# Optimization experiments

Hardware: AMD Instinct MI355X
Metric: run time of the kernel (lower is better)

Reference implementation:

```python
import jax, jax.numpy as jnp
import numpy as np

N = 10000
E = 160000
NEG_SLOPE = 0.2
BN_EPS = 1e-5


def _gat_conv(x, W, a_src, a_dst, b, src, dst, n, heads):
    # PyG GATConv, concat=False (mean over heads), shared lin for src/dst.
    H = heads
    C = W.shape[1] // H
    h = (x @ W).reshape(n, H, C)                       # (N,H,C)
    e_s = jnp.einsum('nhc,hc->nh', h, a_src)           # (N,H)
    e_d = jnp.einsum('nhc,hc->nh', h, a_dst)
    alpha = jax.nn.leaky_relu(e_s[src] + e_d[dst], NEG_SLOPE)   # (E',H)
    amax = jax.ops.segment_max(alpha, dst, num_segments=n)       # per-dst softmax
    ex = jnp.exp(alpha - amax[dst])
    denom = jax.ops.segment_sum(ex, dst, num_segments=n)
    w = ex / (denom[dst] + 1e-16)
    out = jax.ops.segment_sum(h[src] * w[:, :, None], dst, num_segments=n)  # (N,H,C)
    return out.mean(axis=1) + b


def _bn(x, g, b):
    mu = x.mean(axis=0)
    var = x.var(axis=0)  # biased, as torch BN training forward
    return (x - mu) * jax.lax.rsqrt(var + BN_EPS) * g + b


def setup_inputs() -> dict:
    key = jax.random.key(0)
    ks = jax.random.split(key, 32)
    d = {}
    d['x'] = jax.random.normal(ks[0], (N, 64), jnp.float32)
    d['edge_index'] = jax.random.randint(ks[1], (2, E), 0, N, jnp.int64)
    s = lambda k, shape, fan: jax.random.normal(k, shape, jnp.float32) * (1.0 / np.sqrt(fan))
    d['Wp'] = s(ks[2], (64, 128), 64); d['bp'] = jnp.zeros((128,), jnp.float32)
    # conv0: 8 heads, per-head 128
    d['W0'] = s(ks[3], (128, 8 * 128), 128); d['as0'] = s(ks[4], (8, 128), 128)
    d['ad0'] = s(ks[5], (8, 128), 128); d['b0'] = jnp.zeros((128,), jnp.float32)
    d['g0'] = jnp.ones((128,), jnp.float32); d['be0'] = jnp.zeros((128,), jnp.float32)
    # conv1: same shape
    d['W1'] = s(ks[6], (128, 8 * 128), 128); d['as1'] = s(ks[7], (8, 128), 128)
    d['ad1'] = s(ks[8], (8, 128), 128); d['b1'] = jnp.zeros((128,), jnp.float32)
    d['g1'] = jnp.ones((128,), jnp.float32); d['be1'] = jnp.zeros((128,), jnp.float32)
    # conv2: 1 head, out 64
    d['W2'] = s(ks[9], (128, 64), 128); d['as2'] = s(ks[10], (1, 64), 64)
    d['ad2'] = s(ks[11], (1, 64), 64); d['b2'] = jnp.zeros((64,), jnp.float32)
    d['g2'] = jnp.ones((64,), jnp.float32); d['be2'] = jnp.zeros((64,), jnp.float32)
    # residual projection for layer 2 (128 -> 64)
    d['Wr'] = s(ks[12], (128, 64), 128); d['br'] = jnp.zeros((64,), jnp.float32)
    return d


def reference(x, edge_index, Wp, bp, W0, as0, ad0, b0, g0, be0,
              W1, as1, ad1, b1, g1, be1, W2, as2, ad2, b2, g2, be2, Wr, br):
    n = x.shape[0]
    loops = jnp.arange(n, dtype=edge_index.dtype)
    src = jnp.concatenate([edge_index[0], loops])  # add_self_loops=True
    dst = jnp.concatenate([edge_index[1], loops])
    h = x @ Wp + bp
    # layer 0 (8 heads, identity residual)
    hr = h
    h = jax.nn.elu(_bn(_gat_conv(h, W0, as0, ad0, b0, src, dst, n, 8), g0, be0)) + hr
    # layer 1
    hr = h
    h = jax.nn.elu(_bn(_gat_conv(h, W1, as1, ad1, b1, src, dst, n, 8), g1, be1)) + hr
    # layer 2 (1 head, linear residual 128->64)
    hr = h @ Wr + br
    h = jax.nn.elu(_bn(_gat_conv(h, W2, as2, ad2, b2, src, dst, n, 1), g2, be2)) + hr
    return h
```

## Files before the change

### kernel.cpp

```cpp
#include <hip/hip_runtime.h>
#include <hip/hip_bf16.h>
#include <cstdint>
#include <cstddef>

#define TPB 256

typedef __attribute__((ext_vector_type(8))) short bf16x8;
typedef __attribute__((ext_vector_type(8))) unsigned short ushort8;
typedef __attribute__((ext_vector_type(4))) float f32x4;

static __device__ __forceinline__ float bf2f(unsigned short u) {
  union { unsigned int i; float f; } c;
  c.i = ((unsigned int)u) << 16;
  return c.f;
}

__global__ void detect_kernel(const unsigned int* __restrict__ w, int* __restrict__ flag) {
  __shared__ int any32;
  if (threadIdx.x == 0) any32 = 0;
  __syncthreads();
  for (int i = threadIdx.x; i < 1024; i += TPB)
    if (w[2 * i + 1] != 0u) any32 = 1;
  __syncthreads();
  if (threadIdx.x == 0) *flag = any32;
}

__global__ void decode_kernel(const void* __restrict__ raw, const int* __restrict__ flag,
                              int* __restrict__ src, int* __restrict__ dst, int E, int n) {
  int i = blockIdx.x * TPB + threadIdx.x;
  int tot = E + n;
  if (i >= tot) return;
  if (i < E) {
    if (*flag) {
      const int* p = (const int*)raw;
      src[i] = p[i];
      dst[i] = p[E + i];
    } else {
      const long long* p = (const long long*)raw;
      src[i] = (int)p[i];
      dst[i] = (int)p[E + i];
    }
  } else {
    src[i] = i - E;
    dst[i] = i - E;
  }
}

__global__ void count_kernel(const int* __restrict__ dst, int* __restrict__ counts, int etot) {
  int i = blockIdx.x * TPB + threadIdx.x;
  if (i < etot) atomicAdd(&counts[dst[i]], 1);
}

__global__ void scan_kernel(const int* __restrict__ counts, int* __restrict__ row_ptr, int n) {
  __shared__ int part[TPB];
  int tid = threadIdx.x;
  int chunk = (n + TPB - 1) / TPB;
  int begin = tid * chunk;
  int end = begin + chunk; if (end > n) end = n;
  int s = 0;
  for (int i = begin; i < end && i < n; i++) s += counts[i];
  part[tid] = s;
  __syncthreads();
  for (int off = 1; off < TPB; off <<= 1) {
    int v = (tid >= off) ? part[tid - off] : 0;
    __syncthreads();
    part[tid] += v;
    __syncthreads();
  }
  int base = (tid == 0) ? 0 : part[tid - 1];
  for (int i = begin; i < end && i < n; i++) { row_ptr[i] = base; base += counts[i]; }
  if (tid == TPB - 1) row_ptr[n] = base;
}

__global__ void fill_kernel(const int* __restrict__ src, const int* __restrict__ dst,
                            const int* __restrict__ row_ptr, int* __restrict__ fill,
                            int* __restrict__ sorted_src, int etot) {
  int i = blockIdx.x * TPB + threadIdx.x;
  if (i >= etot) return;
  int d = dst[i];
  int pos = row_ptr[d] + atomicAdd(&fill[d], 1);
  sorted_src[pos] = src[i];
}

__global__ void f32_to_bf16_kernel(const float* __restrict__ in, __hip_bfloat16* __restrict__ out, int n) {
  int i = blockIdx.x * TPB + threadIdx.x;
  if (i < n) out[i] = __float2bfloat16(in[i]);
}

__global__ void f32_to_bf16_T_kernel(const float* __restrict__ in, __hip_bfloat16* __restrict__ out,
                                     int K, int N) {
  __shared__ float tile[32][33];
// ... 28 lines not shown
  f32x4 acc[8];
#pragma unroll
  for (int nt = 0; nt < 8; nt++) acc[nt] = (f32x4){0.f, 0.f, 0.f, 0.f};

  const int arow = tid >> 2;
  const int akk = (tid & 3) << 3;
  const int brow = tid >> 1;
  const int bkk = (tid & 1) << 4;

  for (int k0 = 0; k0 < K; k0 += 32) {
    {
      int gr = bm + arow;
      if (gr < M) {
        *(bf16x8*)&As[arow][akk] = *(const bf16x8*)&A[(size_t)gr * K + k0 + akk];
      } else {
        bf16x8 z = {0, 0, 0, 0, 0, 0, 0, 0};
        *(bf16x8*)&As[arow][akk] = z;
      }
    }
    {
      int gbn = bn + brow;
      if (gbn < Ncols) {
        const short* bp = &Bt[(size_t)gbn * K + k0 + bkk];
        *(bf16x8*)&Bs[brow][bkk]     = *(const bf16x8*)bp;
        *(bf16x8*)&Bs[brow][bkk + 8] = *(const bf16x8*)(bp + 8);
      } else {
        bf16x8 z = {0, 0, 0, 0, 0, 0, 0, 0};
        *(bf16x8*)&Bs[brow][bkk] = z;
        *(bf16x8*)&Bs[brow][bkk + 8] = z;
      }
    }
    __syncthreads();

    bf16x8 a = *(const bf16x8*)&As[w * 16 + (lane & 15)][(lane >> 4) * 8];
#pragma unroll
    for (int nt = 0; nt < 8; nt++) {
      bf16x8 b = *(const bf16x8*)&Bs[nt * 16 + (lane & 15)][(lane >> 4) * 8];
      acc[nt] = __builtin_amdgcn_mfma_f32_16x16x32_bf16(a, b, acc[nt], 0, 0, 0);
    }
    __syncthreads();
  }

  float p1[4] = {0.f, 0.f, 0.f, 0.f};
  float p2[4] = {0.f, 0.f, 0.f, 0.f};

#pragma unroll
  for (int nt = 0; nt < 8; nt++) {
    int gc = bn + nt * 16 + (lane & 15);
    if (gc >= Ncols) continue;
    float bv = bias ? bias[gc] : 0.f;
    float asv = es_out ? asrc[gc] : 0.f;
    float adv = es_out ? adst[gc] : 0.f;
#pragma unroll
    for (int q = 0; q < 4; q++) {
      int gr = bm + w * 16 + (lane >> 4) * 4 + q;
      if (gr < M) {
        float val = acc[nt][q] + bv;
        if (C) C[(size_t)gr * Ncols + gc] = val;
        if (Cb) Cb[(size_t)gr * Ncols + gc] = __float2bfloat16(val);
        p1[q] += val * asv;
        p2[q] += val * adv;
      }
    }
  }

  if (es_out) {
    const int head = bn >> hshift;
#pragma unroll
    for (int q = 0; q < 4; q++) {
      float s1 = p1[q], s2 = p2[q];
      s1 += __shfl_xor(s1, 1); s2 += __shfl_xor(s2, 1);
      s1 += __shfl_xor(s1, 2); s2 += __shfl_xor(s2, 2);
      s1 += __shfl_xor(s1, 4); s2 += __shfl_xor(s2, 4);
      s1 += __shfl_xor(s1, 8); s2 += __shfl_xor(s2, 8);
      int gr = bm + w * 16 + (lane >> 4) * 4 + q;
      if ((lane & 15) == 0 && gr < M) {
        es_out[(size_t)gr * H + head] = s1;
        ed_out[(size_t)gr * H + head] = s2;
      }
    }
  }
}

__global__ __launch_bounds__(256) void gat_aggregate8w_kernel(
    const int* __restrict__ row_ptr, const int* __restrict__ srcs,
    const unsigned short* __restrict__ gb, const float* __restrict__ es,
    const float* __restrict__ ed, const float* __restrict__ bias,
    float* __restrict__ out, int n) {
  const int wave = threadIdx.x >> 6;
  const int lane = threadIdx.x & 63;
  const int v = blockIdx.x * 4 + wave;

  __shared__ float wlds[4][64][8];
  __shared__ int slds[4][64];

  if (v >= n) return;

  const int begin = row_ptr[v];
  const int deg = row_ptr[v + 1] - begin;

  const int eh = lane & 7;
  const int ee = lane >> 3;
  const int hh = lane >> 3;
  const int c0 = lane << 4;

  const float edv = ed[(size_t)v * 8 + eh];

  float acc[16];
#pragma unroll
  for (int k = 0; k < 16; k++) acc[k] = 0.f;

  if (deg <= 64) {
    float a[8];
    int sreg[8];
#pragma unroll
    for (int b = 0; b < 8; b++) {
      a[b] = -1e30f;
      sreg[b] = 0;
      int e = b * 8 + ee;
      if (e < deg) {
        int s = srcs[begin + e];
        sreg[b] = s;
        float t = es[(size_t)s * 8 + eh] + edv;
        a[b] = t > 0.f ? t : 0.2f * t;
      }
    }
    float m = a[0];
#pragma unroll
    for (int b = 1; b < 8; b++) m = fmaxf(m, a[b]);
    m = fmaxf(m, __shfl_xor(m, 8));
    m = fmaxf(m, __shfl_xor(m, 16));
    m = fmaxf(m, __shfl_xor(m, 32));
    float dsum = 0.f;
#pragma unroll
    for (int b = 0; b < 8; b++) { a[b] = __expf(a[b] - m); dsum += a[b]; }
    dsum += __shfl_xor(dsum, 8);
    dsum += __shfl_xor(dsum, 16);
    dsum += __shfl_xor(dsum, 32);
    const float invd = 1.0f / (dsum + 1e-16f);
#pragma unroll
    for (int b = 0; b < 8; b++) {
      wlds[wave][b * 8 + ee][eh] = a[b] * invd;
      if (eh == 0) slds[wave][b * 8 + ee] = sreg[b];
    }

    const int npad = (deg + 3) & ~3;
    for (int j0 = 0; j0 < npad; j0 += 4) {
      float w0 = wlds[wave][j0 + 0][hh];
      float w1 = wlds[wave][j0 + 1][hh];
      float w2 = wlds[wave][j0 + 2][hh];
      float w3 = wlds[wave][j0 + 3][hh];
      int s0 = slds[wave][j0 + 0];
      int s1 = slds[wave][j0 + 1];
      int s2 = slds[wave][j0 + 2];
      int s3 = slds[wave][j0 + 3];
      const ushort8* p0 = (const ushort8*)&gb[(size_t)s0 * 1024 + c0];
      const ushort8* p1 = (const ushort8*)&gb[(size_t)s1 * 1024 + c0];
      const ushort8* p2 = (const ushort8*)&gb[(size_t)s2 * 1024 + c0];
      const ushort8* p3 = (const ushort8*)&gb[(size_t)s3 * 1024 + c0];
      ushort8 u0a = p0[0], u0b = p0[1];
      ushort8 u1a = p1[0], u1b = p1[1];
      ushort8 u2a = p2[0], u2b = p2[1];
      ushort8 u3a = p3[0], u3b = p3[1];
#pragma unroll
      for (int k = 0; k < 8; k++) {
        acc[k]     += w0 * bf2f(u0a[k]) + w1 * bf2f(u1a[k]) + w2 * bf2f(u2a[k]) + w3 * bf2f(u3a[k]);
        acc[k + 8] += w0 * bf2f(u0b[k]) + w1 * bf2f(u1b[k]) + w2 * bf2f(u2b[k]) + w3 * bf2f(u3b[k]);
      }
    }
  } else {
    float m = -1e30f;
    for (int base = ee; base < deg; base += 8) {
      int s = srcs[begin + base];
      float t = es[(size_t)s * 8 + eh] + edv;
      t = t > 0.f ? t : 0.2f * t;
      m = fmaxf(m, t);
    }
    m = fmaxf(m, __shfl_xor(m, 8));
    m = fmaxf(m, __shfl_xor(m, 16));
    m = fmaxf(m, __shfl_xor(m, 32));
    float dsum = 0.f;
    for (int base = ee; base < deg; base += 8) {
      int s = srcs[begin + base];
      float t = es[(size_t)s * 8 + eh] + edv;
      t = t > 0.f ? t : 0.2f * t;
      dsum += __expf(t - m);
    }
    dsum += __shfl_xor(dsum, 8);
    dsum += __shfl_xor(dsum, 16);
    dsum += __shfl_xor(dsum, 32);
    const float invd = 1.0f / (dsum + 1e-16f);

    for (int base = 0; base < deg; base += 64) {
      const int cnt = min(64, deg - base);
#pragma unroll
      for (int b = 0; b < 8; b++) {
        int e = base + b * 8 + ee;
        float wv = 0.f;
        int s = 0;
        if (e < deg) {
          s = srcs[begin + e];
          float t = es[(size_t)s * 8 + eh] + edv;
          t = t > 0.f ? t : 0.2f * t;
          wv = __expf(t - m) * invd;
        }
        wlds[wave][b * 8 + ee][eh] = wv;
        if (eh == 0) slds[wave][b * 8 + ee] = s;
      }
      const int npad = (cnt + 3) & ~3;
      for (int j0 = 0; j0 < npad; j0 += 4) {
        float w0 = wlds[wave][j0 + 0][hh];
        float w1 = wlds[wave][j0 + 1][hh];
        float w2 = wlds[wave][j0 + 2][hh];
        float w3 = wlds[wave][j0 + 3][hh];
        int s0 = slds[wave][j0 + 0];
        int s1 = slds[wave][j0 + 1];
        int s2 = slds[wave][j0 + 2];
        int s3 = slds[wave][j0 + 3];
        const ushort8* p0 = (const ushort8*)&gb[(size_t)s0 * 1024 + c0];
        const ushort8* p1 = (const ushort8*)&gb[(size_t)s1 * 1024 + c0];
        const ushort8* p2 = (const ushort8*)&gb[(size_t)s2 * 1024 + c0];
        const ushort8* p3 = (const ushort8*)&gb[(size_t)s3 * 1024 + c0];
        ushort8 u0a = p0[0], u0b = p0[1];
        ushort8 u1a = p1[0], u1b = p1[1];
        ushort8 u2a = p2[0], u2b = p2[1];
        ushort8 u3a = p3[0], u3b = p3[1];
#pragma unroll
        for (int k = 0; k < 8; k++) {
          acc[k]     += w0 * bf2f(u0a[k]) + w1 * bf2f(u1a[k]) + w2 * bf2f(u2a[k]) + w3 * bf2f(u3a[k]);
          acc[k + 8] += w0 * bf2f(u0b[k]) + w1 * bf2f(u1b[k]) + w2 * bf2f(u2b[k]) + w3 * bf2f(u3b[k]);
        }
      }
    }
  }

#pragma unroll
  for (int k = 0; k < 16; k++) {
    acc[k] += __shfl_xor(acc[k], 8);
    acc[k] += __shfl_xor(acc[k], 16);
    acc[k] += __shfl_xor(acc[k], 32);
  }
  if (hh == 0) {
    const int cc = (lane & 7) << 4;
#pragma unroll
    for (int k = 0; k < 16; k++)
      out[(size_t)v * 128 + cc + k] = acc[k] * 0.125f + bias[cc + k];
  }
}

__global__ __launch_bounds__(256) void gat_aggregate1_kernel(
    const int* __restrict__ row_ptr, const int* __restrict__ srcs,
    const float* __restrict__ g, const float* __restrict__ es,
    const float* __restrict__ ed, const float* __restrict__ bias,
    float* __restrict__ out, int n) {
  const int wave = threadIdx.x >> 6;
  const int lane = threadIdx.x & 63;
  const int v = blockIdx.x * 4 + wave;
  if (v >= n) return;

  const int begin = row_ptr[v];
  const int deg = row_ptr[v + 1] - begin;
  const float edv = ed[v];

  float pm = -1e30f;
  for (int j = lane; j < deg; j += 64) {
    float a = es[srcs[begin + j]] + edv;
    a = a > 0.f ? a : 0.2f * a;
    pm = fmaxf(pm, a);
  }
#pragma unroll
  for (int off = 32; off > 0; off >>= 1) pm = fmaxf(pm, __shfl_xor(pm, off));

  float ps = 0.f;
  for (int j = lane; j < deg; j += 64) {
    float a = es[srcs[begin + j]] + edv;
    a = a > 0.f ? a : 0.2f * a;
    ps += expf(a - pm);
  }
#pragma unroll
  for (int off = 32; off > 0; off >>= 1) ps += __shfl_xor(ps, off);
  const float invd = 1.0f / (ps + 1e-16f);

  float acc = 0.f;
  for (int base = 0; base < deg; base += 64) {
    int cnt = deg - base; if (cnt > 64) cnt = 64;
    int sv = 0; float wv = 0.f;
    if (lane < cnt) {
      sv = srcs[begin + base + lane];
      float a = es[sv] + edv;
      a = a > 0.f ? a : 0.2f * a;
      wv = expf(a - pm) * invd;
    }
    for (int j = 0; j < cnt; j++) {
      int s = __shfl(sv, j);
      float wgt = __shfl(wv, j);
      acc += wgt * g[(size_t)s * 64 + lane];
    }
  }
  out[(size_t)v * 64 + lane] = acc + bias[lane];
}

template <int C>
__global__ void bn_stats_kernel(const float* __restrict__ x, int n, float* __restrict__ sums) {
  constexpr int T = 256;
  constexpr int RPI = T / C;
  constexpr int ITER = 64;
  constexpr int ROWS = RPI * ITER;
  int c = threadIdx.x % C;
  int r0 = threadIdx.x / C;
  int rowBase = blockIdx.x * ROWS;
  float s = 0.f, q = 0.f;
  for (int it = 0; it < ITER; ++it) {
    int r = rowBase + it * RPI + r0;
    if (r < n) {
      float v = x[(size_t)r * C + c];
      s += v; q += v * v;
    }
  }
  __shared__ float ls[T], lq[T];
  ls[threadIdx.x] = s; lq[threadIdx.x] = q;
  __syncthreads();
  if (threadIdx.x < C) {
    float ts = 0.f, tq = 0.f;
    for (int r = 0; r < RPI; ++r) { ts += ls[c + r * C]; tq += lq[c + r * C]; }
    atomicAdd(&sums[c], ts);
    atomicAdd(&sums[C + c], tq);
  }
}

template <int C>
__global__ void bn_elu_res_kernel(const float* __restrict__ x, const float* __restrict__ sums,
                                  const float* __restrict__ gamma, const float* __restrict__ beta,
                                  const float* __restrict__ res, float* __restrict__ out,
                                  __hip_bfloat16* __restrict__ outb, int n) {
  int i = blockIdx.x * TPB + threadIdx.x;
  if (i >= n * C) return;
  int c = i % C;
  float inv_n = 1.0f / (float)n;
  float mu = sums[c] * inv_n;
  float var = sums[C + c] * inv_n - mu * mu;
  float y = (x[i] - mu) * rsqrtf(var + 1e-5f) * gamma[c] + beta[c];
  y = y > 0.f ? y : expm1f(y);
  y += res[i];
  out[i] = y;
  if (outb) outb[i] = __float2bfloat16(y);
}

extern "C" void kernel_launch(void* const* d_in, const int* in_sizes, int n_in,
                              void* d_out, int out_size, void* d_ws, size_t ws_size,
                              hipStream_t stream) {
  const float* x   = (const float*)d_in[0];
  const void*  ei  = d_in[1];
  const float* Wp  = (const float*)d_in[2];
  const float* bp  = (const float*)d_in[3];
  const float* W0  = (const float*)d_in[4];
  const float* as0 = (const float*)d_in[5];
  const float* ad0 = (const float*)d_in[6];
  const float* b0  = (const float*)d_in[7];
  const float* g0  = (const float*)d_in[8];
  const float* be0 = (const float*)d_in[9];
  const float* W1  = (const float*)d_in[10];
  const float* as1 = (const float*)d_in[11];
  const float* ad1 = (const float*)d_in[12];
  const float* b1  = (const float*)d_in[13];
  const float* g1  = (const float*)d_in[14];
  const float* be1 = (const float*)d_in[15];
  const float* W2  = (const float*)d_in[16];
  const float* as2 = (const float*)d_in[17];
  const float* ad2 = (const float*)d_in[18];
  const float* b2  = (const float*)d_in[19];
  const float* g2  = (const float*)d_in[20];
  const float* be2 = (const float*)d_in[21];
  const float* Wr  = (const float*)d_in[22];
  const float* br  = (const float*)d_in[23];

  const int N = in_sizes[0] / 64;
  const int E = in_sizes[1] / 2;
  const int ETOT = E + N;

  char* wsp = (char*)d_ws;
  size_t off = 0;
  auto alloc = [&](size_t bytes) -> void* {
    void* p = wsp + off;
    off += (bytes + 255) & ~(size_t)255;
    return p;
  };
  int*   flag    = (int*)alloc(4);
  int*   e_src   = (int*)alloc((size_t)ETOT * 4);
  int*   e_dst   = (int*)alloc((size_t)ETOT * 4);
  int*   counts  = (int*)alloc((size_t)N * 4);
  int*   fillc   = (int*)alloc((size_t)N * 4);
  int*   row_ptr = (int*)alloc((size_t)(N + 1) * 4);
  int*   s_src   = (int*)alloc((size_t)ETOT * 4);
  float* hA      = (float*)alloc((size_t)N * 128 * 4);
  float* hB      = (float*)alloc((size_t)N * 128 * 4);
  float* gbuf    = (float*)alloc((size_t)N * 64 * 4);
  float* gat     = (float*)alloc((size_t)N * 128 * 4);
  float* es      = (float*)alloc((size_t)N * 8 * 4);
  float* ed      = (float*)alloc((size_t)N * 8 * 4);
  float* bnsum   = (float*)alloc(2 * 128 * 4);
  __hip_bfloat16* gbufb = (__hip_bfloat16*)alloc((size_t)N * 1024 * 2);
  __hip_bfloat16* xb  = (__hip_bfloat16*)alloc((size_t)N * 64 * 2);
  __hip_bfloat16* hAb = (__hip_bfloat16*)alloc((size_t)N * 128 * 2);
  __hip_bfloat16* hBb = (__hip_bfloat16*)alloc((size_t)N * 128 * 2);
  __hip_bfloat16* WpT = (__hip_bfloat16*)alloc((size_t)128 * 64 * 2);
  __hip_bfloat16* W0T = (__hip_bfloat16*)alloc((size_t)1024 * 128 * 2);
  __hip_bfloat16* W1T = (__hip_bfloat16*)alloc((size_t)1024 * 128 * 2);
  __hip_bfloat16* W2T = (__hip_bfloat16*)alloc((size_t)64 * 128 * 2);
  __hip_bfloat16* WrT = (__hip_bfloat16*)alloc((size_t)64 * 128 * 2);

  const int egrid = (ETOT + TPB - 1) / TPB;
  const int mgrid = (N + 63) / 64;
  auto cgrid = [](int n) { return (n + TPB - 1) / TPB; };

  detect_kernel<<<1, TPB, 0, stream>>>((const unsigned int*)ei, flag);
  decode_kernel<<<egrid, TPB, 0, stream>>>(ei, flag, e_src, e_dst, E, N);
  hipMemsetAsync(counts, 0, (size_t)N * 4, stream);
  hipMemsetAsync(fillc, 0, (size_t)N * 4, stream);
  count_kernel<<<egrid, TPB, 0, stream>>>(e_dst, counts, ETOT);
  scan_kernel<<<1, TPB, 0, stream>>>(counts, row_ptr, N);
  fill_kernel<<<egrid, TPB, 0, stream>>>(e_src, e_dst, row_ptr, fillc, s_src, ETOT);

  f32_to_bf16_kernel<<<cgrid(N * 64), TPB, 0, stream>>>(x, xb, N * 64);
  f32_to_bf16_T_kernel<<<dim3(2, 4), 256, 0, stream>>>(Wp, WpT, 64, 128);
  f32_to_bf16_T_kernel<<<dim3(4, 32), 256, 0, stream>>>(W0, W0T, 128, 1024);
  f32_to_bf16_T_kernel<<<dim3(4, 32), 256, 0, stream>>>(W1, W1T, 128, 1024);
  f32_to_bf16_T_kernel<<<dim3(4, 2), 256, 0, stream>>>(W2, W2T, 128, 64);
  f32_to_bf16_T_kernel<<<dim3(4, 2), 256, 0, stream>>>(Wr, WrT, 128, 64);

  gemm_bf16t_kernel<<<dim3(mgrid, 1), 256, 0, stream>>>(
      (const short*)xb, (const short*)WpT, bp, hA, hAb, N, 128, 64,
      nullptr, nullptr, nullptr, nullptr, 1, 7);

  gemm_bf16t_kernel<<<dim3(mgrid, 8), 256, 0, stream>>>(
      (const short*)hAb, (const short*)W0T, nullptr, nullptr, gbufb, N, 1024, 128,
      as0, ad0, es, ed, 8, 7);
  gat_aggregate8w_kernel<<<(N + 3) / 4, 256, 0, stream>>>(
      row_ptr, s_src, (const unsigned short*)gbufb, es, ed, b0, gat, N);
  hipMemsetAsync(bnsum, 0, 2 * 128 * 4, stream);
  bn_stats_kernel<128><<<(N + 127) / 128, 256, 0, stream>>>(gat, N, bnsum);
  bn_elu_res_kernel<128><<<cgrid(N * 128), TPB, 0, stream>>>(gat, bnsum, g0, be0, hA, hB, hBb, N);

  gemm_bf16t_kernel<<<dim3(mgrid, 8), 256, 0, stream>>>(
      (const short*)hBb, (const short*)W1T, nullptr, nullptr, gbufb, N, 1024, 128,
      as1, ad1, es, ed, 8, 7);
  gat_aggregate8w_kernel<<<(N + 3) / 4, 256, 0, stream>>>(
      row_ptr, s_src, (const unsigned short*)gbufb, es, ed, b1, gat, N);
  hipMemsetAsync(bnsum, 0, 2 * 128 * 4, stream);
  bn_stats_kernel<128><<<(N + 127) / 128, 256, 0, stream>>>(gat, N, bnsum);
  bn_elu_res_kernel<128><<<cgrid(N * 128), TPB, 0, stream>>>(gat, bnsum, g1, be1, hB, hA, hAb, N);

  gemm_bf16t_kernel<<<dim3(mgrid, 1), 256, 0, stream>>>(
      (const short*)hAb, (const short*)WrT, br, hB, nullptr, N, 64, 128,
      nullptr, nullptr, nullptr, nullptr, 1, 7);
  gemm_bf16t_kernel<<<dim3(mgrid, 1), 256, 0, stream>>>(
      (const short*)hAb, (const short*)W2T, nullptr, gbuf, nullptr, N, 64, 128,
      as2, ad2, es, ed, 1, 6);
  gat_aggregate1_kernel<<<(N + 3) / 4, 256, 0, stream>>>(row_ptr, s_src, gbuf, es, ed, b2, gat, N);
  hipMemsetAsync(bnsum, 0, 2 * 64 * 4, stream);
  bn_stats_kernel<64><<<(N + 255) / 256, 256, 0, stream>>>(gat, N, bnsum);
  bn_elu_res_kernel<64><<<cgrid(N * 64), TPB, 0, stream>>>(gat, bnsum, g2, be2, hB, (float*)d_out, nullptr, N);
}
```

Measured before the change: 321.2 us.

## Split 8-head GAT aggregation across two waves per node, 4 heads each

The 8-head aggregation kernel now assigns two waves per destination node, each handling four heads (512 bf16 columns), so each lane accumulates 8 values instead of 16. The gather loop is unrolled to eight neighbours per step with a tree-shaped sum, and the two half-node partials are combined through shared memory after a block barrier. This aims to double the parallelism and memory-level concurrency of the gather-bound aggregation and to cut register pressure. It adds an LDS exchange and __syncthreads, and inactive waves must stay alive until the barrier. The single-head kernel also switches expf to __expf.

Result: no change. 319.8 us (-0.4%).

```diff
diff --git a/kernel.cpp b/kernel.cpp
--- a/kernel.cpp
+++ b/kernel.cpp
@@ -206,105 +206,113 @@
     const unsigned short* __restrict__ gb, const float* __restrict__ es,
     const float* __restrict__ ed, const float* __restrict__ bias,
     float* __restrict__ out, int n) {
-  const int wave = threadIdx.x >> 6;
+  const int wg = threadIdx.x >> 6;
   const int lane = threadIdx.x & 63;
-  const int v = blockIdx.x * 4 + wave;
-
-  __shared__ float wlds[4][64][8];
+  const int v = blockIdx.x * 2 + (wg >> 1);
+  const int w = wg & 1;
+
+  __shared__ float wlds[4][64][4];
   __shared__ int slds[4][64];
-
-  if (v >= n) return;
-
-  const int begin = row_ptr[v];
-  const int deg = row_ptr[v + 1] - begin;
-
-  const int eh = lane & 7;
-  const int ee = lane >> 3;
-  const int hh = lane >> 3;
-  const int c0 = lane << 4;
-
-  const float edv = ed[(size_t)v * 8 + eh];
-
-  float acc[16];
-#pragma unroll
-  for (int k = 0; k < 16; k++) acc[k] = 0.f;
-
-  if (deg <= 64) {
-    float a[8];
-    int sreg[8];
-#pragma unroll
-    for (int b = 0; b < 8; b++) {
+  __shared__ float plds[4][16][8];
+
+  const bool active = (v < n);
+  const int begin = active ? row_ptr[v] : 0;
+  const int deg = active ? (row_ptr[v + 1] - begin) : 0;
+
+  const int eh4 = lane & 3;
+  const int ee16 = lane >> 2;
+  const int hh4 = lane >> 4;
+  const int c0 = w * 512 + lane * 8;
+
+  const float edv = active ? ed[(size_t)v * 8 + w * 4 + eh4] : 0.f;
+
+  float acc[8];
+#pragma unroll
+  for (int k = 0; k < 8; k++) acc[k] = 0.f;
+
+  if (active && deg <= 64) {
+    float a[4];
+    int sreg[4];
+#pragma unroll
+    for (int b = 0; b < 4; b++) {
       a[b] = -1e30f;
       sreg[b] = 0;
-      int e = b * 8 + ee;
+      int e = b * 16 + ee16;
       if (e < deg) {
         int s = srcs[begin + e];
         sreg[b] = s;
-        float t = es[(size_t)s * 8 + eh] + edv;
+        float t = es[(size_t)s * 8 + w * 4 + eh4] + edv;
         a[b] = t > 0.f ? t : 0.2f * t;
       }
     }
-    float m = a[0];
-#pragma unroll
-    for (int b = 1; b < 8; b++) m = fmaxf(m, a[b]);
+    float m = fmaxf(fmaxf(a[0], a[1]), fmaxf(a[2], a[3]));
+    m = fmaxf(m, __shfl_xor(m, 4));
     m = fmaxf(m, __shfl_xor(m, 8));
     m = fmaxf(m, __shfl_xor(m, 16));
     m = fmaxf(m, __shfl_xor(m, 32));
     float dsum = 0.f;
 #pragma unroll
-    for (int b = 0; b < 8; b++) { a[b] = __expf(a[b] - m); dsum += a[b]; }
+    for (int b = 0; b < 4; b++) { a[b] = __expf(a[b] - m); dsum += a[b]; }
+    dsum += __shfl_xor(dsum, 4);
     dsum += __shfl_xor(dsum, 8);
     dsum += __shfl_xor(dsum, 16);
     dsum += __shfl_xor(dsum, 32);
     const float invd = 1.0f / (dsum + 1e-16f);
 #pragma unroll
-    for (int b = 0; b < 8; b++) {
-      wlds[wave][b * 8 + ee][eh] = a[b] * invd;
-      if (eh == 0) slds[wave][b * 8 + ee] = sreg[b];
-    }
-
-    const int npad = (deg + 3) & ~3;
-    for (int j0 = 0; j0 < npad; j0 += 4) {
-      float w0 = wlds[wave][j0 + 0][hh];
-      float w1 = wlds[wave][j0 + 1][hh];
-      float w2 = wlds[wave][j0 + 2][hh];
-      float w3 = wlds[wave][j0 + 3][hh];
-      int s0 = slds[wave][j0 + 0];
-      int s1 = slds[wave][j0 + 1];
-      int s2 = slds[wave][j0 + 2];
-      int s3 = slds[wave][j0 + 3];
-      const ushort8* p0 = (const ushort8*)&gb[(size_t)s0 * 1024 + c0];
-      const ushort8* p1 = (const ushort8*)&gb[(size_t)s1 * 1024 + c0];
-      const ushort8* p2 = (const ushort8*)&gb[(size_t)s2 * 1024 + c0];
-      const ushort8* p3 = (const ushort8*)&gb[(size_t)s3 * 1024 + c0];
-      ushort8 u0a = p0[0], u0b = p0[1];
-      ushort8 u1a = p1[0], u1b = p1[1];
-      ushort8 u2a = p2[0], u2b = p2[1];
-      ushort8 u3a = p3[0], u3b = p3[1];
+    for (int b = 0; b < 4; b++) {
+      wlds[wg][b * 16 + ee16][eh4] = a[b] * invd;
+      if (eh4 == 0) slds[wg][b * 16 + ee16] = sreg[b];
+    }
+
+#pragma unroll
+    for (int g8 = 0; g8 < 8; g8++) {
+      const int j0 = g8 * 8;
+      if (j0 >= deg) break;
+      float w0 = wlds[wg][j0 + 0][hh4], w1 = wlds[wg][j0 + 1][hh4];
+      float w2 = wlds[wg][j0 + 2][hh4], w3 = wlds[wg][j0 + 3][hh4];
+      float w4 = wlds[wg][j0 + 4][hh4], w5 = wlds[wg][j0 + 5][hh4];
+      float w6 = wlds[wg][j0 + 6][hh4], w7 = wlds[wg][j0 + 7][hh4];
+      int s0 = slds[wg][j0 + 0], s1 = slds[wg][j0 + 1];
+      int s2 = slds[wg][j0 + 2], s3 = slds[wg][j0 + 3];
+      int s4 = slds[wg][j0 + 4], s5 = slds[wg][j0 + 5];
+      int s6 = slds[wg][j0 + 6], s7 = slds[wg][j0 + 7];
+      ushort8 u0 = *(const ushort8*)&gb[(size_t)s0 * 1024 + c0];
+      ushort8 u1 = *(const ushort8*)&gb[(size_t)s1 * 1024 + c0];
+      ushort8 u2 = *(const ushort8*)&gb[(size_t)s2 * 1024 + c0];
+      ushort8 u3 = *(const ushort8*)&gb[(size_t)s3 * 1024 + c0];
+      ushort8 u4 = *(const ushort8*)&gb[(size_t)s4 * 1024 + c0];
+      ushort8 u5 = *(const ushort8*)&gb[(size_t)s5 * 1024 + c0];
+      ushort8 u6 = *(const ushort8*)&gb[(size_t)s6 * 1024 + c0];
+      ushort8 u7 = *(const ushort8*)&gb[(size_t)s7 * 1024 + c0];
 #pragma unroll
       for (int k = 0; k < 8; k++) {
-        acc[k]     += w0 * bf2f(u0a[k]) + w1 * bf2f(u1a[k]) + w2 * bf2f(u2a[k]) + w3 * bf2f(u3a[k]);
-        acc[k + 8] += w0 * bf2f(u0b[k]) + w1 * bf2f(u1b[k]) + w2 * bf2f(u2b[k]) + w3 * bf2f(u3b[k]);
-      }
-    }
-  } else {
+        float t0 = w0 * bf2f(u0[k]) + w1 * bf2f(u1[k]);
+        float t1 = w2 * bf2f(u2[k]) + w3 * bf2f(u3[k]);
+        float t2 = w4 * bf2f(u4[k]) + w5 * bf2f(u5[k]);
+        float t3 = w6 * bf2f(u6[k]) + w7 * bf2f(u7[k]);
+        acc[k] += (t0 + t1) + (t2 + t3);
+      }
+    }
+  } else if (active) {
     float m = -1e30f;
-    for (int base = ee; base < deg; base += 8) {
-      int s = srcs[begin + base];
-      float t = es[(size_t)s * 8 + eh] + edv;
+    for (int e = ee16; e < deg; e += 16) {
+      int s = srcs[begin + e];
+      float t = es[(size_t)s * 8 + w * 4 + eh4] + edv;
       t = t > 0.f ? t : 0.2f * t;
       m = fmaxf(m, t);
     }
+    m = fmaxf(m, __shfl_xor(m, 4));
     m = fmaxf(m, __shfl_xor(m, 8));
     m = fmaxf(m, __shfl_xor(m, 16));
     m = fmaxf(m, __shfl_xor(m, 32));
     float dsum = 0.f;
-    for (int base = ee; base < deg; base += 8) {
-      int s = srcs[begin + base];
-      float t = es[(size_t)s * 8 + eh] + edv;
+    for (int e = ee16; e < deg; e += 16) {
+      int s = srcs[begin + e];
+      float t = es[(size_t)s * 8 + w * 4 + eh4] + edv;
       t = t > 0.f ? t : 0.2f * t;
       dsum += __expf(t - m);
     }
+    dsum += __shfl_xor(dsum, 4);
     dsum += __shfl_xor(dsum, 8);
     dsum += __shfl_xor(dsum, 16);
     dsum += __shfl_xor(dsum, 32);
@@ -313,57 +321,67 @@
     for (int base = 0; base < deg; base += 64) {
       const int cnt = min(64, deg - base);
 #pragma unroll
-      for (int b = 0; b < 8; b++) {
-        int e = base + b * 8 + ee;
-        float wv = 0.f;
-        int s = 0;
+      for (int b = 0; b < 4; b++) {
+        int e = base + b * 16 + ee16;
+        float wv = 0.f; int s = 0;
         if (e < deg) {
           s = srcs[begin + e];
-          float t = es[(size_t)s * 8 + eh] + edv;
+          float t = es[(size_t)s * 8 + w * 4 + eh4] + edv;
           t = t > 0.f ? t : 0.2f * t;
           wv = __expf(t - m) * invd;
         }
-        wlds[wave][b * 8 + ee][eh] = wv;
-        if (eh == 0) slds[wave][b * 8 + ee] = s;
-      }
-      const int npad = (cnt + 3) & ~3;
-      for (int j0 = 0; j0 < npad; j0 += 4) {
-        float w0 = wlds[wave][j0 + 0][hh];
-        float w1 = wlds[wave][j0 + 1][hh];
-        float w2 = wlds[wave][j0 + 2][hh];
-        float w3 = wlds[wave][j0 + 3][hh];
-        int s0 = slds[wave][j0 + 0];
-        int s1 = slds[wave][j0 + 1];
-        int s2 = slds[wave][j0 + 2];
-        int s3 = slds[wave][j0 + 3];
-        const ushort8* p0 = (const ushort8*)&gb[(size_t)s0 * 1024 + c0];
-        const ushort8* p1 = (const ushort8*)&gb[(size_t)s1 * 1024 + c0];
-        const ushort8* p2 = (const ushort8*)&gb[(size_t)s2 * 1024 + c0];
-        const ushort8* p3 = (const ushort8*)&gb[(size_t)s3 * 1024 + c0];
-        ushort8 u0a = p0[0], u0b = p0[1];
-        ushort8 u1a = p1[0], u1b = p1[1];
-        ushort8 u2a = p2[0], u2b = p2[1];
-        ushort8 u3a = p3[0], u3b = p3[1];
+        wlds[wg][b * 16 + ee16][eh4] = wv;
+        if (eh4 == 0) slds[wg][b * 16 + ee16] = s;
+      }
+#pragma unroll
+      for (int g8 = 0; g8 < 8; g8++) {
+        const int j0 = g8 * 8;
+        if (j0 >= cnt) break;
+        float w0 = wlds[wg][j0 + 0][hh4], w1 = wlds[wg][j0 + 1][hh4];
+        float w2 = wlds[wg][j0 + 2][hh4], w3 = wlds[wg][j0 + 3][hh4];
+        float w4 = wlds[wg][j0 + 4][hh4], w5 = wlds[wg][j0 + 5][hh4];
+        float w6 = wlds[wg][j0 + 6][hh4], w7 = wlds[wg][j0 + 7][hh4];
+        int s0 = slds[wg][j0 + 0], s1 = slds[wg][j0 + 1];
+        int s2 = slds[wg][j0 + 2], s3 = slds[wg][j0 + 3];
+        int s4 = slds[wg][j0 + 4], s5 = slds[wg][j0 + 5];
+        int s6 = slds[wg][j0 + 6], s7 = slds[wg][j0 + 7];
+        ushort8 u0 = *(const ushort8*)&gb[(size_t)s0 * 1024 + c0];
+        ushort8 u1 = *(const ushort8*)&gb[(size_t)s1 * 1024 + c0];
+        ushort8 u2 = *(const ushort8*)&gb[(size_t)s2 * 1024 + c0];
+        ushort8 u3 = *(const ushort8*)&gb[(size_t)s3 * 1024 + c0];
+        ushort8 u4 = *(const ushort8*)&gb[(size_t)s4 * 1024 + c0];
+        ushort8 u5 = *(const ushort8*)&gb[(size_t)s5 * 1024 + c0];
+        ushort8 u6 = *(const ushort8*)&gb[(size_t)s6 * 1024 + c0];
+        ushort8 u7 = *(const ushort8*)&gb[(size_t)s7 * 1024 + c0];
 #pragma unroll
         for (int k = 0; k < 8; k++) {
-          acc[k]     += w0 * bf2f(u0a[k]) + w1 * bf2f(u1a[k]) + w2 * bf2f(u2a[k]) + w3 * bf2f(u3a[k]);
-          acc[k + 8] += w0 * bf2f(u0b[k]) + w1 * bf2f(u1b[k]) + w2 * bf2f(u2b[k]) + w3 * bf2f(u3b[k]);
+          float t0 = w0 * bf2f(u0[k]) + w1 * bf2f(u1[k]);
+          float t1 = w2 * bf2f(u2[k]) + w3 * bf2f(u3[k]);
+          float t2 = w4 * bf2f(u4[k]) + w5 * bf2f(u5[k]);
+          float t3 = w6 * bf2f(u6[k]) + w7 * bf2f(u7[k]);
+          acc[k] += (t0 + t1) + (t2 + t3);
         }
       }
     }
   }
 
 #pragma unroll
-  for (int k = 0; k < 16; k++) {
-    acc[k] += __shfl_xor(acc[k], 8);
+  for (int k = 0; k < 8; k++) {
     acc[k] += __shfl_xor(acc[k], 16);
     acc[k] += __shfl_xor(acc[k], 32);
   }
-  if (hh == 0) {
-    const int cc = (lane & 7) << 4;
-#pragma unroll
-    for (int k = 0; k < 16; k++)
-      out[(size_t)v * 128 + cc + k] = acc[k] * 0.125f + bias[cc + k];
+  if (lane < 16) {
+#pragma unroll
+    for (int k = 0; k < 8; k++) plds[wg][lane][k] = acc[k];
+  }
+  __syncthreads();
+  if (active && w == 0 && lane < 16) {
+    const int cc = lane * 8;
+#pragma unroll
+    for (int k = 0; k < 8; k++) {
+      float sum = plds[wg][lane][k] + plds[wg + 1][lane][k];
+      out[(size_t)v * 128 + cc + k] = sum * 0.125f + bias[cc + k];
+    }
   }
 }
 
@@ -394,7 +412,7 @@
   for (int j = lane; j < deg; j += 64) {
     float a = es[srcs[begin + j]] + edv;
     a = a > 0.f ? a : 0.2f * a;
-    ps += expf(a - pm);
+    ps += __expf(a - pm);
   }
 #pragma unroll
   for (int off = 32; off > 0; off >>= 1) ps += __shfl_xor(ps, off);
@@ -408,7 +426,7 @@
       sv = srcs[begin + base + lane];
       float a = es[sv] + edv;
       a = a > 0.f ? a : 0.2f * a;
-      wv = expf(a - pm) * invd;
+      wv = __expf(a - pm) * invd;
     }
     for (int j = 0; j < cnt; j++) {
       int s = __shfl(sv, j);
@@ -554,7 +572,7 @@
   gemm_bf16t_kernel<<<dim3(mgrid, 8), 256, 0, stream>>>(
       (const short*)hAb, (const short*)W0T, nullptr, nullptr, gbufb, N, 1024, 128,
       as0, ad0, es, ed, 8, 7);
-  gat_aggregate8w_kernel<<<(N + 3) / 4, 256, 0, stream>>>(
+  gat_aggregate8w_kernel<<<(N + 1) / 2, 256, 0, stream>>>(
       row_ptr, s_src, (const unsigned short*)gbufb, es, ed, b0, gat, N);
   hipMemsetAsync(bnsum, 0, 2 * 128 * 4, stream);
   bn_stats_kernel<128><<<(N + 127) / 128, 256, 0, stream>>>(gat, N, bnsum);
@@ -563,7 +581,7 @@
   gemm_bf16t_kernel<<<dim3(mgrid, 8), 256, 0, stream>>>(
       (const short*)hBb, (const short*)W1T, nullptr, nullptr, gbufb, N, 1024, 128,
       as1, ad1, es, ed, 8, 7);
-  gat_aggregate8w_kernel<<<(N + 3) / 4, 256, 0, stream>>>(
+  gat_aggregate8w_kernel<<<(N + 1) / 2, 256, 0, stream>>>(
       row_ptr, s_src, (const unsigned short*)gbufb, es, ed, b1, gat, N);
   hipMemsetAsync(bnsum, 0, 2 * 128 * 4, stream);
   bn_stats_kernel<128><<<(N + 127) / 128, 256, 0, stream>>>(gat, N, bnsum);
```

## Split 8-head GAT aggregation into weight, per-head gather and reduce kernels

Applied to the files above, without the earlier changes.

Replaces the fused 8-head aggregation with three kernels. The first computes the softmax attention weights into a per-head edge buffer. The second gathers per head, with blocks partitioned by head and node range so each block touches only a 256-byte head slice of the feature table, meant to improve cache locality. The third sums the bf16 per-head partials. It also rewrites the single-head aggregation to stage weights in LDS and unroll the gather 8-wide, and raises the parallelism of the BN stats kernel; these changes add extra global round-trips through the weight and partial buffers.

Measured after the change: 390.7 us. 1.22x slower.

```diff
diff --git a/kernel.cpp b/kernel.cpp
--- a/kernel.cpp
+++ b/kernel.cpp
@@ -6,7 +6,6 @@
 #define TPB 256
 
 typedef __attribute__((ext_vector_type(8))) short bf16x8;
-typedef __attribute__((ext_vector_type(8))) unsigned short ushort8;
 typedef __attribute__((ext_vector_type(4))) float f32x4;
 
 static __device__ __forceinline__ float bf2f(unsigned short u) {
@@ -201,45 +200,25 @@
   }
 }
 
-__global__ __launch_bounds__(256) void gat_aggregate8w_kernel(
+__global__ __launch_bounds__(256) void gat_weights_kernel(
     const int* __restrict__ row_ptr, const int* __restrict__ srcs,
-    const unsigned short* __restrict__ gb, const float* __restrict__ es,
-    const float* __restrict__ ed, const float* __restrict__ bias,
-    float* __restrict__ out, int n) {
-  const int wave = threadIdx.x >> 6;
-  const int lane = threadIdx.x & 63;
+    const float* __restrict__ es, const float* __restrict__ ed,
+    float* __restrict__ wbuf, int etot, int n) {
+  const int wave = threadIdx.x >> 6, lane = threadIdx.x & 63;
   const int v = blockIdx.x * 4 + wave;
-
-  __shared__ float wlds[4][64][8];
-  __shared__ int slds[4][64];
-
   if (v >= n) return;
-
-  const int begin = row_ptr[v];
-  const int deg = row_ptr[v + 1] - begin;
-
-  const int eh = lane & 7;
-  const int ee = lane >> 3;
-  const int hh = lane >> 3;
-  const int c0 = lane << 4;
-
+  const int begin = row_ptr[v], deg = row_ptr[v + 1] - begin;
+  const int eh = lane & 7, ee = lane >> 3;
   const float edv = ed[(size_t)v * 8 + eh];
-
-  float acc[16];
-#pragma unroll
-  for (int k = 0; k < 16; k++) acc[k] = 0.f;
 
   if (deg <= 64) {
     float a[8];
-    int sreg[8];
 #pragma unroll
     for (int b = 0; b < 8; b++) {
       a[b] = -1e30f;
-      sreg[b] = 0;
       int e = b * 8 + ee;
       if (e < deg) {
         int s = srcs[begin + e];
-        sreg[b] = s;
         float t = es[(size_t)s * 8 + eh] + edv;
         a[b] = t > 0.f ? t : 0.2f * t;
       }
@@ -259,38 +238,13 @@
     const float invd = 1.0f / (dsum + 1e-16f);
 #pragma unroll
     for (int b = 0; b < 8; b++) {
-      wlds[wave][b * 8 + ee][eh] = a[b] * invd;
-      if (eh == 0) slds[wave][b * 8 + ee] = sreg[b];
-    }
-
-    const int npad = (deg + 3) & ~3;
-    for (int j0 = 0; j0 < npad; j0 += 4) {
-      float w0 = wlds[wave][j0 + 0][hh];
-      float w1 = wlds[wave][j0 + 1][hh];
-      float w2 = wlds[wave][j0 + 2][hh];
-      float w3 = wlds[wave][j0 + 3][hh];
-      int s0 = slds[wave][j0 + 0];
-      int s1 = slds[wave][j0 + 1];
-      int s2 = slds[wave][j0 + 2];
-      int s3 = slds[wave][j0 + 3];
-      const ushort8* p0 = (const ushort8*)&gb[(size_t)s0 * 1024 + c0];
-      const ushort8* p1 = (const ushort8*)&gb[(size_t)s1 * 1024 + c0];
-      const ushort8* p2 = (const ushort8*)&gb[(size_t)s2 * 1024 + c0];
-      const ushort8* p3 = (const ushort8*)&gb[(size_t)s3 * 1024 + c0];
-      ushort8 u0a = p0[0], u0b = p0[1];
-      ushort8 u1a = p1[0], u1b = p1[1];
-      ushort8 u2a = p2[0], u2b = p2[1];
-      ushort8 u3a = p3[0], u3b = p3[1];
-#pragma unroll
-      for (int k = 0; k < 8; k++) {
-        acc[k]     += w0 * bf2f(u0a[k]) + w1 * bf2f(u1a[k]) + w2 * bf2f(u2a[k]) + w3 * bf2f(u3a[k]);
-        acc[k + 8] += w0 * bf2f(u0b[k]) + w1 * bf2f(u1b[k]) + w2 * bf2f(u2b[k]) + w3 * bf2f(u3b[k]);
-      }
+      int e = b * 8 + ee;
+      if (e < deg) wbuf[(size_t)eh * etot + begin + e] = a[b] * invd;
     }
   } else {
     float m = -1e30f;
-    for (int base = ee; base < deg; base += 8) {
-      int s = srcs[begin + base];
+    for (int e = ee; e < deg; e += 8) {
+      int s = srcs[begin + e];
       float t = es[(size_t)s * 8 + eh] + edv;
       t = t > 0.f ? t : 0.2f * t;
       m = fmaxf(m, t);
@@ -299,8 +253,8 @@
     m = fmaxf(m, __shfl_xor(m, 16));
     m = fmaxf(m, __shfl_xor(m, 32));
     float dsum = 0.f;
-    for (int base = ee; base < deg; base += 8) {
-      int s = srcs[begin + base];
+    for (int e = ee; e < deg; e += 8) {
+      int s = srcs[begin + e];
       float t = es[(size_t)s * 8 + eh] + edv;
       t = t > 0.f ? t : 0.2f * t;
       dsum += __expf(t - m);
@@ -309,62 +263,80 @@
     dsum += __shfl_xor(dsum, 16);
     dsum += __shfl_xor(dsum, 32);
     const float invd = 1.0f / (dsum + 1e-16f);
-
-    for (int base = 0; base < deg; base += 64) {
-      const int cnt = min(64, deg - base);
-#pragma unroll
-      for (int b = 0; b < 8; b++) {
-        int e = base + b * 8 + ee;
-        float wv = 0.f;
-        int s = 0;
-        if (e < deg) {
-          s = srcs[begin + e];
-          float t = es[(size_t)s * 8 + eh] + edv;
-          t = t > 0.f ? t : 0.2f * t;
-          wv = __expf(t - m) * invd;
-        }
-        wlds[wave][b * 8 + ee][eh] = wv;
-        if (eh == 0) slds[wave][b * 8 + ee] = s;
-      }
-      const int npad = (cnt + 3) & ~3;
-      for (int j0 = 0; j0 < npad; j0 += 4) {
-        float w0 = wlds[wave][j0 + 0][hh];
-        float w1 = wlds[wave][j0 + 1][hh];
-        float w2 = wlds[wave][j0 + 2][hh];
-        float w3 = wlds[wave][j0 + 3][hh];
-        int s0 = slds[wave][j0 + 0];
-        int s1 = slds[wave][j0 + 1];
-        int s2 = slds[wave][j0 + 2];
-        int s3 = slds[wave][j0 + 3];
-        const ushort8* p0 = (const ushort8*)&gb[(size_t)s0 * 1024 + c0];
-        const ushort8* p1 = (const ushort8*)&gb[(size_t)s1 * 1024 + c0];
-        const ushort8* p2 = (const ushort8*)&gb[(size_t)s2 * 1024 + c0];
-        const ushort8* p3 = (const ushort8*)&gb[(size_t)s3 * 1024 + c0];
-        ushort8 u0a = p0[0], u0b = p0[1];
-        ushort8 u1a = p1[0], u1b = p1[1];
-        ushort8 u2a = p2[0], u2b = p2[1];
-        ushort8 u3a = p3[0], u3b = p3[1];
-#pragma unroll
-        for (int k = 0; k < 8; k++) {
-          acc[k]     += w0 * bf2f(u0a[k]) + w1 * bf2f(u1a[k]) + w2 * bf2f(u2a[k]) + w3 * bf2f(u3a[k]);
-          acc[k + 8] += w0 * bf2f(u0b[k]) + w1 * bf2f(u1b[k]) + w2 * bf2f(u2b[k]) + w3 * bf2f(u3b[k]);
-        }
-      }
-    }
-  }
-
-#pragma unroll
-  for (int k = 0; k < 16; k++) {
-    acc[k] += __shfl_xor(acc[k], 8);
-    acc[k] += __shfl_xor(acc[k], 16);
-    acc[k] += __shfl_xor(acc[k], 32);
-  }
-  if (hh == 0) {
-    const int cc = (lane & 7) << 4;
-#pragma unroll
-    for (int k = 0; k < 16; k++)
-      out[(size_t)v * 128 + cc + k] = acc[k] * 0.125f + bias[cc + k];
-  }
+    for (int e = ee; e < deg; e += 8) {
+      int s = srcs[begin + e];
+      float t = es[(size_t)s * 8 + eh] + edv;
+      t = t > 0.f ? t : 0.2f * t;
+      wbuf[(size_t)eh * etot + begin + e] = __expf(t - m) * invd;
+    }
+  }
+}
+
+__global__ __launch_bounds__(256) void gat_gather_head_kernel(
+    const int* __restrict__ row_ptr, const int* __restrict__ srcs,
+    const unsigned short* __restrict__ gb, const float* __restrict__ wbuf,
+    unsigned short* __restrict__ partial, int etot, int n, int nb) {
+  const int h = blockIdx.x & 7;
+  const int nblk = blockIdx.x >> 3;
+  const int wave = threadIdx.x >> 6, lane = threadIdx.x & 63;
+  const int per = (n + nb - 1) / nb;
+  const int v1 = min((nblk + 1) * per, n);
+  const float* wb = wbuf + (size_t)h * etot;
+  const unsigned short* gsl = gb + h * 128;
+  unsigned short* pout = partial + (size_t)h * n * 128;
+  const int c = lane * 2;
+
+  for (int v = nblk * per + wave; v < v1; v += 4) {
+    const int begin = row_ptr[v];
+    const int deg = row_ptr[v + 1] - begin;
+    float ax = 0.f, ay = 0.f;
+    for (int base = 0; base < deg; base += 8) {
+      int e = base + (lane & 7);
+      int sv = 0; float wv = 0.f;
+      if (e < deg) { sv = srcs[begin + e]; wv = wb[begin + e]; }
+      int s0 = __shfl(sv, 0), s1 = __shfl(sv, 1), s2 = __shfl(sv, 2), s3 = __shfl(sv, 3);
+      int s4 = __shfl(sv, 4), s5 = __shfl(sv, 5), s6 = __shfl(sv, 6), s7 = __shfl(sv, 7);
+      float w0 = __shfl(wv, 0), w1 = __shfl(wv, 1), w2 = __shfl(wv, 2), w3 = __shfl(wv, 3);
+      float w4 = __shfl(wv, 4), w5 = __shfl(wv, 5), w6 = __shfl(wv, 6), w7 = __shfl(wv, 7);
+      unsigned int u0 = *(const unsigned int*)&gsl[(size_t)s0 * 1024 + c];
+      unsigned int u1 = *(const unsigned int*)&gsl[(size_t)s1 * 1024 + c];
+      unsigned int u2 = *(const unsigned int*)&gsl[(size_t)s2 * 1024 + c];
+      unsigned int u3 = *(const unsigned int*)&gsl[(size_t)s3 * 1024 + c];
+      unsigned int u4 = *(const unsigned int*)&gsl[(size_t)s4 * 1024 + c];
+      unsigned int u5 = *(const unsigned int*)&gsl[(size_t)s5 * 1024 + c];
+      unsigned int u6 = *(const unsigned int*)&gsl[(size_t)s6 * 1024 + c];
+      unsigned int u7 = *(const unsigned int*)&gsl[(size_t)s7 * 1024 + c];
+      ax += w0 * bf2f((unsigned short)u0) + w1 * bf2f((unsigned short)u1)
+          + w2 * bf2f((unsigned short)u2) + w3 * bf2f((unsigned short)u3)
+          + w4 * bf2f((unsigned short)u4) + w5 * bf2f((unsigned short)u5)
+          + w6 * bf2f((unsigned short)u6) + w7 * bf2f((unsigned short)u7);
+      ay += w0 * bf2f((unsigned short)(u0 >> 16)) + w1 * bf2f((unsigned short)(u1 >> 16))
+          + w2 * bf2f((unsigned short)(u2 >> 16)) + w3 * bf2f((unsigned short)(u3 >> 16))
+          + w4 * bf2f((unsigned short)(u4 >> 16)) + w5 * bf2f((unsigned short)(u5 >> 16))
+          + w6 * bf2f((unsigned short)(u6 >> 16)) + w7 * bf2f((unsigned short)(u7 >> 16));
+    }
+    __hip_bfloat16 bx = __float2bfloat16(ax), by = __float2bfloat16(ay);
+    unsigned int o = (unsigned int)*(unsigned short*)&bx
+                   | ((unsigned int)*(unsigned short*)&by << 16);
+    *(unsigned int*)&pout[(size_t)v * 128 + c] = o;
+  }
+}
+
+__global__ void gat_reduce_kernel(const unsigned short* __restrict__ partial,
+                                  const float* __restrict__ bias,
+                                  float* __restrict__ out, int n) {
+  int idx = blockIdx.x * TPB + threadIdx.x;
+  if (idx >= n * 64) return;
+  int v = idx >> 6, c = (idx & 63) * 2;
+  float sx = 0.f, sy = 0.f;
+#pragma unroll
+  for (int h = 0; h < 8; h++) {
+    unsigned int u = *(const unsigned int*)&partial[(size_t)h * n * 128 + (size_t)v * 128 + c];
+    sx += bf2f((unsigned short)u);
+    sy += bf2f((unsigned short)(u >> 16));
+  }
+  out[(size_t)v * 128 + c]     = sx * 0.125f + bias[c];
+  out[(size_t)v * 128 + c + 1] = sy * 0.125f + bias[c + 1];
 }
 
 __global__ __launch_bounds__(256) void gat_aggregate1_kernel(
@@ -375,45 +347,109 @@
   const int wave = threadIdx.x >> 6;
   const int lane = threadIdx.x & 63;
   const int v = blockIdx.x * 4 + wave;
+
+  __shared__ float wlds[4][64];
+  __shared__ int slds[4][64];
+
   if (v >= n) return;
 
   const int begin = row_ptr[v];
   const int deg = row_ptr[v + 1] - begin;
   const float edv = ed[v];
 
-  float pm = -1e30f;
-  for (int j = lane; j < deg; j += 64) {
-    float a = es[srcs[begin + j]] + edv;
-    a = a > 0.f ? a : 0.2f * a;
-    pm = fmaxf(pm, a);
-  }
-#pragma unroll
-  for (int off = 32; off > 0; off >>= 1) pm = fmaxf(pm, __shfl_xor(pm, off));
-
-  float ps = 0.f;
-  for (int j = lane; j < deg; j += 64) {
-    float a = es[srcs[begin + j]] + edv;
-    a = a > 0.f ? a : 0.2f * a;
-    ps += expf(a - pm);
-  }
-#pragma unroll
-  for (int off = 32; off > 0; off >>= 1) ps += __shfl_xor(ps, off);
-  const float invd = 1.0f / (ps + 1e-16f);
-
   float acc = 0.f;
-  for (int base = 0; base < deg; base += 64) {
-    int cnt = deg - base; if (cnt > 64) cnt = 64;
-    int sv = 0; float wv = 0.f;
-    if (lane < cnt) {
-      sv = srcs[begin + base + lane];
-      float a = es[sv] + edv;
+
+  if (deg <= 64) {
+    float a = -1e30f;
+    int s = 0;
+    if (lane < deg) {
+      s = srcs[begin + lane];
+      float t = es[s] + edv;
+      a = t > 0.f ? t : 0.2f * t;
+    }
+    float m = a;
+#pragma unroll
+    for (int off = 32; off > 0; off >>= 1) m = fmaxf(m, __shfl_xor(m, off));
+    float p = __expf(a - m);
+    float dsum = p;
+#pragma unroll
+    for (int off = 32; off > 0; off >>= 1) dsum += __shfl_xor(dsum, off);
+    const float invd = 1.0f / (dsum + 1e-16f);
+    wlds[wave][lane] = p * invd;
+    slds[wave][lane] = s;
+
+    const int npad = (deg + 7) & ~7;
+    for (int j0 = 0; j0 < npad; j0 += 8) {
+      float w0 = wlds[wave][j0 + 0], w1 = wlds[wave][j0 + 1];
+      float w2 = wlds[wave][j0 + 2], w3 = wlds[wave][j0 + 3];
+      float w4 = wlds[wave][j0 + 4], w5 = wlds[wave][j0 + 5];
+      float w6 = wlds[wave][j0 + 6], w7 = wlds[wave][j0 + 7];
+      int s0 = slds[wave][j0 + 0], s1 = slds[wave][j0 + 1];
+      int s2 = slds[wave][j0 + 2], s3 = slds[wave][j0 + 3];
+      int s4 = slds[wave][j0 + 4], s5 = slds[wave][j0 + 5];
+      int s6 = slds[wave][j0 + 6], s7 = slds[wave][j0 + 7];
+      float f0 = g[(size_t)s0 * 64 + lane];
+      float f1 = g[(size_t)s1 * 64 + lane];
+      float f2 = g[(size_t)s2 * 64 + lane];
+      float f3 = g[(size_t)s3 * 64 + lane];
+      float f4 = g[(size_t)s4 * 64 + lane];
+      float f5 = g[(size_t)s5 * 64 + lane];
+      float f6 = g[(size_t)s6 * 64 + lane];
+      float f7 = g[(size_t)s7 * 64 + lane];
+      acc += (w0 * f0 + w1 * f1) + (w2 * f2 + w3 * f3)
+           + (w4 * f4 + w5 * f5) + (w6 * f6 + w7 * f7);
+    }
+  } else {
+    float pm = -1e30f;
+    for (int j = lane; j < deg; j += 64) {
+      float a = es[srcs[begin + j]] + edv;
       a = a > 0.f ? a : 0.2f * a;
-      wv = expf(a - pm) * invd;
-    }
-    for (int j = 0; j < cnt; j++) {
-      int s = __shfl(sv, j);
-      float wgt = __shfl(wv, j);
-      acc += wgt * g[(size_t)s * 64 + lane];
+      pm = fmaxf(pm, a);
+    }
+#pragma unroll
+    for (int off = 32; off > 0; off >>= 1) pm = fmaxf(pm, __shfl_xor(pm, off));
+    float ps = 0.f;
+    for (int j = lane; j < deg; j += 64) {
+      float a = es[srcs[begin + j]] + edv;
+      a = a > 0.f ? a : 0.2f * a;
+      ps += __expf(a - pm);
+    }
+#pragma unroll
+    for (int off = 32; off > 0; off >>= 1) ps += __shfl_xor(ps, off);
+    const float invd = 1.0f / (ps + 1e-16f);
+
+    for (int base = 0; base < deg; base += 64) {
+      int cnt = min(64, deg - base);
+      float wv = 0.f; int s = 0;
+      if (lane < cnt) {
+        s = srcs[begin + base + lane];
+        float a = es[s] + edv;
+        a = a > 0.f ? a : 0.2f * a;
+        wv = __expf(a - pm) * invd;
+      }
+      wlds[wave][lane] = wv;
+      slds[wave][lane] = s;
+      const int npad = (cnt + 7) & ~7;
+      for (int j0 = 0; j0 < npad; j0 += 8) {
+        float w0 = wlds[wave][j0 + 0], w1 = wlds[wave][j0 + 1];
+        float w2 = wlds[wave][j0 + 2], w3 = wlds[wave][j0 + 3];
+        float w4 = wlds[wave][j0 + 4], w5 = wlds[wave][j0 + 5];
+        float w6 = wlds[wave][j0 + 6], w7 = wlds[wave][j0 + 7];
+        int s0 = slds[wave][j0 + 0], s1 = slds[wave][j0 + 1];
+        int s2 = slds[wave][j0 + 2], s3 = slds[wave][j0 + 3];
+        int s4 = slds[wave][j0 + 4], s5 = slds[wave][j0 + 5];
+        int s6 = slds[wave][j0 + 6], s7 = slds[wave][j0 + 7];
+        float f0 = g[(size_t)s0 * 64 + lane];
+        float f1 = g[(size_t)s1 * 64 + lane];
+        float f2 = g[(size_t)s2 * 64 + lane];
+        float f3 = g[(size_t)s3 * 64 + lane];
+        float f4 = g[(size_t)s4 * 64 + lane];
+        float f5 = g[(size_t)s5 * 64 + lane];
+        float f6 = g[(size_t)s6 * 64 + lane];
+        float f7 = g[(size_t)s7 * 64 + lane];
+        acc += (w0 * f0 + w1 * f1) + (w2 * f2 + w3 * f3)
+             + (w4 * f4 + w5 * f5) + (w6 * f6 + w7 * f7);
+      }
     }
   }
   out[(size_t)v * 64 + lane] = acc + bias[lane];
@@ -423,7 +459,7 @@
 __global__ void bn_stats_kernel(const float* __restrict__ x, int n, float* __restrict__ sums) {
   constexpr int T = 256;
   constexpr int RPI = T / C;
-  constexpr int ITER = 64;
+  constexpr int ITER = 8;
   constexpr int ROWS = RPI * ITER;
   int c = threadIdx.x % C;
   int r0 = threadIdx.x / C;
@@ -513,12 +549,14 @@
   int*   s_src   = (int*)alloc((size_t)ETOT * 4);
   float* hA      = (float*)alloc((size_t)N * 128 * 4);
   float* hB      = (float*)alloc((size_t)N * 128 * 4);
-  float* gbuf    = (float*)alloc((size_t)N * 64 * 4);
   float* gat     = (float*)alloc((size_t)N * 128 * 4);
   float* es      = (float*)alloc((size_t)N * 8 * 4);
   float* ed      = (float*)alloc((size_t)N * 8 * 4);
   float* bnsum   = (float*)alloc(2 * 128 * 4);
+  float* wbuf    = (float*)alloc((size_t)ETOT * 8 * 4);
   __hip_bfloat16* gbufb = (__hip_bfloat16*)alloc((size_t)N * 1024 * 2);
+  float* gbuf    = (float*)gbufb;
+  unsigned short* partial = (unsigned short*)alloc((size_t)N * 1024 * 2);
   __hip_bfloat16* xb  = (__hip_bfloat16*)alloc((size_t)N * 64 * 2);
   __hip_bfloat16* hAb = (__hip_bfloat16*)alloc((size_t)N * 128 * 2);
   __hip_bfloat16* hBb = (__hip_bfloat16*)alloc((size_t)N * 128 * 2);
@@ -530,6 +568,7 @@
 
   const int egrid = (ETOT + TPB - 1) / TPB;
   const int mgrid = (N + 63) / 64;
+  const int NB = 64;
   auto cgrid = [](int n) { return (n + TPB - 1) / TPB; };
 
   detect_kernel<<<1, TPB, 0, stream>>>((const unsigned int*)ei, flag);
@@ -554,19 +593,23 @@
   gemm_bf16t_kernel<<<dim3(mgrid, 8), 256, 0, stream>>>(
       (const short*)hAb, (const short*)W0T, nullptr, nullptr, gbufb, N, 1024, 128,
       as0, ad0, es, ed, 8, 7);
-  gat_aggregate8w_kernel<<<(N + 3) / 4, 256, 0, stream>>>(
-      row_ptr, s_src, (const unsigned short*)gbufb, es, ed, b0, gat, N);
+  gat_weights_kernel<<<(N + 3) / 4, 256, 0, stream>>>(row_ptr, s_src, es, ed, wbuf, ETOT, N);
+  gat_gather_head_kernel<<<8 * NB, 256, 0, stream>>>(
+      row_ptr, s_src, (const unsigned short*)gbufb, wbuf, partial, ETOT, N, NB);
+  gat_reduce_kernel<<<cgrid(N * 64), TPB, 0, stream>>>(partial, b0, gat, N);
   hipMemsetAsync(bnsum, 0, 2 * 128 * 4, stream);
-  bn_stats_kernel<128><<<(N + 127) / 128, 256, 0, stream>>>(gat, N, bnsum);
+  bn_stats_kernel<128><<<(N + 15) / 16, 256, 0, stream>>>(gat, N, bnsum);
   bn_elu_res_kernel<128><<<cgrid(N * 128), TPB, 0, stream>>>(gat, bnsum, g0, be0, hA, hB, hBb, N);
 
   gemm_bf16t_kernel<<<dim3(mgrid, 8), 256, 0, stream>>>(
       (const short*)hBb, (const short*)W1T, nullptr, nullptr, gbufb, N, 1024, 128,
       as1, ad1, es, ed, 8, 7);
-  gat_aggregate8w_kernel<<<(N + 3) / 4, 256, 0, stream>>>(
-      row_ptr, s_src, (const unsigned short*)gbufb, es, ed, b1, gat, N);
+  gat_weights_kernel<<<(N + 3) / 4, 256, 0, stream>>>(row_ptr, s_src, es, ed, wbuf, ETOT, N);
+  gat_gather_head_kernel<<<8 * NB, 256, 0, stream>>>(
+      row_ptr, s_src, (const unsigned short*)gbufb, wbuf, partial, ETOT, N, NB);
+  gat_reduce_kernel<<<cgrid(N * 64), TPB, 0, stream>>>(partial, b1, gat, N);
   hipMemsetAsync(bnsum, 0, 2 * 128 * 4, stream);
-  bn_stats_kernel<128><<<(N + 127) / 128, 256, 0, stream>>>(gat, N, bnsum);
+  bn_stats_kernel<128><<<(N + 15) / 16, 256, 0, stream>>>(gat, N, bnsum);
   bn_elu_res_kernel<128><<<cgrid(N * 128), TPB, 0, stream>>>(gat, bnsum, g1, be1, hB, hA, hAb, N);
 
   gemm_bf16t_kernel<<<dim3(mgrid, 1), 256, 0, stream>>>(
@@ -577,6 +620,6 @@
       as2, ad2, es, ed, 1, 6);
   gat_aggregate1_kernel<<<(N + 3) / 4, 256, 0, stream>>>(row_ptr, s_src, gbuf, es, ed, b2, gat, N);
   hipMemsetAsync(bnsum, 0, 2 * 64 * 4, stream);
-  bn_stats_kernel<64><<<(N + 255) / 256, 256, 0, stream>>>(gat, N, bnsum);
+  bn_stats_kernel<64><<<(N + 31) / 32, 256, 0, stream>>>(gat, N, bnsum);
   bn_elu_res_kernel<64><<<cgrid(N * 64), TPB, 0, stream>>>(gat, bnsum, g2, be2, hB, (float*)d_out, nullptr, N);
 }
```
